# Kernel tuning notes

Measured on AMD Instinct MI355X. Metric: run time of the kernel, lower is better.

## Reference

```python
import jax, jax.numpy as jnp
import numpy as np

D_MODEL = 1024
N_HEADS = 16
MAX_LAG = 512
D_K = D_MODEL // N_HEADS


def setup_inputs() -> dict:
    key = jax.random.key(0)
    ks = jax.random.split(key, 11)
    B, S = 2, 2048
    x = jax.random.normal(ks[0], (B, S, D_MODEL), dtype=jnp.float32)
    lag = jax.random.randint(ks[1], (S,), 0, MAX_LAG + 1, dtype=jnp.int64)
    scale = 1.0 / np.sqrt(D_MODEL)
    wq = jax.random.normal(ks[2], (D_MODEL, D_MODEL), dtype=jnp.float32) * scale
    bq = jnp.zeros((D_MODEL,), dtype=jnp.float32)
    wk = jax.random.normal(ks[3], (D_MODEL, D_MODEL), dtype=jnp.float32) * scale
    bk = jnp.zeros((D_MODEL,), dtype=jnp.float32)
    wv = jax.random.normal(ks[4], (D_MODEL, D_MODEL), dtype=jnp.float32) * scale
    bv = jnp.zeros((D_MODEL,), dtype=jnp.float32)
    wo = jax.random.normal(ks[5], (D_MODEL, D_MODEL), dtype=jnp.float32) * scale
    bo = jnp.zeros((D_MODEL,), dtype=jnp.float32)
    lag_bias = jax.random.normal(ks[6], (N_HEADS, MAX_LAG + 1), dtype=jnp.float32) * 0.02
    return {"x": x, "lag": lag, "wq": wq, "bq": bq, "wk": wk, "bk": bk,
            "wv": wv, "bv": bv, "wo": wo, "bo": bo, "lag_bias": lag_bias}


def reference(x, lag, wq, bq, wk, bk, wv, bv, wo, bo, lag_bias):
    B, S, D = x.shape
    H, dk = N_HEADS, D_K
    # projections: torch Linear is x @ W.T + b; here weights stored as (in, out)
    q = (x @ wq + bq).reshape(B, S, H, dk).transpose(0, 2, 1, 3)  # (B,H,S,dk)
    k = (x @ wk + bk).reshape(B, S, H, dk).transpose(0, 2, 1, 3)
    v = (x @ wv + bv).reshape(B, S, H, dk).transpose(0, 2, 1, 3)
    scores = jnp.einsum('bhqd,bhkd->bhqk', q, k) / jnp.sqrt(jnp.float32(dk))
    ld = jnp.abs(lag[:, None] - lag[None, :]).astype(jnp.int32)  # (S,S)
    bias = lag_bias[:, ld]  # (H,S,S)
    attn = jax.nn.softmax(scores + bias[None], axis=-1)
    out = jnp.einsum('bhqk,bhkd->bhqd', attn, v)
    out = out.transpose(0, 2, 1, 3).reshape(B, S, D)
    return out @ wo + bo
```

## Files before the change

### kernel.cpp

```cpp
#include <hip/hip_runtime.h>

typedef __bf16 bf16;
typedef __bf16 bf16x8 __attribute__((ext_vector_type(8)));
typedef float f32x4 __attribute__((ext_vector_type(4)));

__device__ __forceinline__ f32x4 mfma16(bf16x8 a, bf16x8 b, f32x4 c) {
  return __builtin_amdgcn_mfma_f32_16x16x32_bf16(a, b, c, 0, 0, 0);
}
__device__ __forceinline__ void gload16(const bf16* g, bf16* l) {
  __builtin_amdgcn_global_load_lds((const __attribute__((address_space(1))) unsigned int*)g,
                                   (__attribute__((address_space(3))) unsigned int*)l, 16, 0, 0);
}

__global__ __launch_bounds__(256) void cvt_x_kernel(const float* __restrict__ in,
                                                    bf16* __restrict__ out, int n8) {
  int i = blockIdx.x * 256 + threadIdx.x;
  if (i >= n8) return;
  const float4* p = (const float4*)in + (size_t)i * 2;
  float4 f0 = p[0], f1 = p[1];
  bf16x8 o;
  o[0] = (bf16)f0.x; o[1] = (bf16)f0.y; o[2] = (bf16)f0.z; o[3] = (bf16)f0.w;
  o[4] = (bf16)f1.x; o[5] = (bf16)f1.y; o[6] = (bf16)f1.z; o[7] = (bf16)f1.w;
  *((bf16x8*)out + i) = o;
}

__global__ __launch_bounds__(256) void cvt_wtb_kernel(
    const float* __restrict__ wq, const float* __restrict__ wk,
    const float* __restrict__ wv, const float* __restrict__ wo,
    const float* __restrict__ bq, const float* __restrict__ bk,
    const float* __restrict__ bv, bf16* __restrict__ wqkvt,
    bf16* __restrict__ wot, float* __restrict__ bqkv) {
  int blk = blockIdx.x;
  int tid = threadIdx.x;
  if (blk >= 1024) {
    int i = (blk - 1024) * 256 + tid;
    if (i < 1024) bqkv[i] = bq[i];
    else if (i < 2048) bqkv[i] = bk[i - 1024];
    else if (i < 3072) bqkv[i] = bv[i - 2048];
    return;
  }
  __shared__ float t[64][68];
  int wsel = blk >> 8, sub = blk & 255;
  const float* in = wsel == 0 ? wq : wsel == 1 ? wk : wsel == 2 ? wv : wo;
  bf16* out = (wsel == 3) ? wot : (wqkvt + (size_t)wsel * (1u << 20));
  int bx = sub & 15;
  int by = sub >> 4;
  int r = tid >> 2, p = tid & 3;
  const float* src = in + (size_t)(by * 64 + r) * 1024 + bx * 64 + p * 16;
#pragma unroll
  for (int j = 0; j < 16; j += 4)
    *(float4*)&t[r][p * 16 + j] = *(const float4*)(src + j);
  __syncthreads();
  int n = tid >> 2, sp = tid & 3;
  bf16 tmp[16];
#pragma unroll
  for (int j = 0; j < 16; ++j) tmp[j] = (bf16)t[sp * 16 + j][n];
  bf16* dst = out + (size_t)(bx * 64 + n) * 1024 + by * 64 + sp * 16;
  *(bf16x8*)dst = *(bf16x8*)&tmp[0];
  *(bf16x8*)(dst + 8) = *(bf16x8*)&tmp[8];
}

__global__ __launch_bounds__(256) void sort_lag_kernel(const int* __restrict__ lag,
                                                       int* __restrict__ perm,
                                                       int* __restrict__ slag) {
  __shared__ int l[2048];
  int tid = threadIdx.x;
  for (int i = tid; i < 2048; i += 256) l[i] = lag[i];
  __syncthreads();
  int i = blockIdx.x * 32 + (tid >> 3);
  int s = tid & 7;
  int vi = l[i];
  int cnt = 0;
  for (int j = s * 256; j < s * 256 + 256; j += 4) {
    int4 vj = *(const int4*)&l[j];
    cnt += (vj.x < vi || (vj.x == vi && (j + 0) < i));
    cnt += (vj.y < vi || (vj.y == vi && (j + 1) < i));
    cnt += (vj.z < vi || (vj.z == vi && (j + 2) < i));
    cnt += (vj.w < vi || (vj.w == vi && (j + 3) < i));
  }
  cnt += __shfl_xor(cnt, 1);
  cnt += __shfl_xor(cnt, 2);
  cnt += __shfl_xor(cnt, 4);
  if (s == 0) { perm[cnt] = i; slag[cnt] = vi; }
}

__global__ __launch_bounds__(256) void pack_kv_kernel(const bf16* __restrict__ qkv,
                                                      const int* __restrict__ perm,
                                                      bf16* __restrict__ kp,
                                                      bf16* __restrict__ vt) {
  __shared__ bf16 t[64][72];
  int blk = blockIdx.x;
  int st = blk & 31, h = (blk >> 5) & 15, b = blk >> 9;
  int tid = threadIdx.x;
  int r = tid >> 2, p = tid & 3;
  int src_s = perm[st * 64 + r];
  {
    const bf16* src = qkv + (size_t)(b * 2048 + src_s) * 3072 + 1024 + h * 64 + p * 16;
    bf16* dst = kp + (size_t)((b * 16 + h) * 2048 + st * 64 + r) * 64 + p * 16;
    *(bf16x8*)dst = *(const bf16x8*)src;
    *(bf16x8*)(dst + 8) = *(const bf16x8*)(src + 8);
  }
  {
    const bf16* src = qkv + (size_t)(b * 2048 + src_s) * 3072 + 2048 + h * 64 + p * 16;
    *(bf16x8*)&t[r][p * 16] = *(const bf16x8*)src;
    *(bf16x8*)&t[r][p * 16 + 8] = *(const bf16x8*)(src + 8);
    __syncthreads();
    int d = tid >> 2, sp = tid & 3;
    bf16 tmp[16];
#pragma unroll
    for (int j = 0; j < 16; ++j) tmp[j] = t[sp * 16 + j][d];
    bf16* dst = vt + (size_t)((b * 16 + h) * 64 + d) * 2048 + st * 64 + sp * 16;
    *(bf16x8*)dst = *(bf16x8*)&tmp[0];
    *(bf16x8*)(dst + 8) = *(bf16x8*)&tmp[8];
  }
}

template <int OUT_BF16>
__global__ __launch_bounds__(256) void gemm_bt_kernel(
    const bf16* __restrict__ A, const bf16* __restrict__ Bt,
    const float* __restrict__ bias, void* __restrict__ C,
    int M, int N, int K, int scale_cols, float scale_val) {
  __shared__ __align__(16) bf16 As[128 * 64];
  __shared__ __align__(16) bf16 Bs[128 * 64];
  int bn = blockIdx.x * 128, bm = blockIdx.y * 128;
  int tid = threadIdx.x;
  int l = tid & 63;
  int w = tid >> 6;
  int wr = w >> 1, wc = w & 1;
  int g = l >> 4, c = l & 15;
  int swz = (c & 7) << 3;
  int srow = l >> 3;
  int scol = ((l & 7) ^ srow) << 3;
  const bf16* Ap = A + (size_t)(bm + w * 32 + srow) * K + scol;
  const bf16* Bp = Bt + (size_t)(bn + w * 32 + srow) * K + scol;
  bf16* AsW = As + w * 32 * 64;
  bf16* BsW = Bs + w * 32 * 64;

  f32x4 acc[4][4] = {};
  for (int k0 = 0; k0 < K; k0 += 64) {
    __syncthreads();
#pragma unroll
    for (int i = 0; i < 4; ++i) {
      gload16(Ap + (size_t)(8 * i) * K + k0, AsW + i * 512);
      gload16(Bp + (size_t)(8 * i) * K + k0, BsW + i * 512);
    }
    __syncthreads();
#pragma unroll
    for (int kh = 0; kh < 2; ++kh) {
      bf16x8 af[4], bfr[4];
#pragma unroll
      for (int m = 0; m < 4; ++m)
        af[m] = *(const bf16x8*)&As[(wr * 64 + m * 16 + c) * 64 + ((kh * 32 + g * 8) ^ swz)];
#pragma unroll
      for (int n = 0; n < 4; ++n)
        bfr[n] = *(const bf16x8*)&Bs[(wc * 64 + n * 16 + c) * 64 + ((kh * 32 + g * 8) ^ swz)];
#pragma unroll
      for (int m = 0; m < 4; ++m)
#pragma unroll
        for (int n = 0; n < 4; ++n)
          acc[m][n] = mfma16(af[m], bfr[n], acc[m][n]);
    }
  }
  int rowb = bm + wr * 64;
  int colb = bn + wc * 64;
#pragma unroll
  for (int n = 0; n < 4; ++n) {
    int col = colb + n * 16 + c;
    float bv = bias[col];
    float s = (col < scale_cols) ? scale_val : 1.0f;
#pragma unroll
    for (int m = 0; m < 4; ++m) {
      int row = rowb + m * 16 + g * 4;
#pragma unroll
      for (int j = 0; j < 4; ++j) {
        float v = (acc[m][n][j] + bv) * s;
        if (OUT_BF16)
          ((bf16*)C)[(size_t)(row + j) * N + col] = (bf16)v;
        else
          ((float*)C)[(size_t)(row + j) * N + col] = v;
      }
    }
  }
}

__global__ __launch_bounds__(256) void attn_kernel(
    const bf16* __restrict__ qkv, const bf16* __restrict__ kp,
    const bf16* __restrict__ vt, const int* __restrict__ lag,
    const int* __restrict__ slag, const float* __restrict__ lag_bias,
    bf16* __restrict__ out) {
  __shared__ __align__(16) bf16 Ks0[64 * 64];
  __shared__ __align__(16) bf16 Vs0[64 * 64];
  __shared__ __align__(16) bf16 Ks1[64 * 64];
  __shared__ __align__(16) bf16 Vs1[64 * 64];
  __shared__ __align__(16) bf16 Ps[4][16][72];
  __shared__ float bias_s[516];
  __shared__ int lag_s[2048];

  int blk = blockIdx.x;
  blk = (blk & 7) * 128 + (blk >> 3);
  int qt = blk & 31;
  int h = (blk >> 5) & 15;
  int b = blk >> 9;
  int tid = threadIdx.x;
  int w = tid >> 6, l = tid & 63, g = l >> 4, c = l & 15;

  for (int i = tid; i < 513; i += 256) bias_s[i] = lag_bias[h * 513 + i] * 1.44269504f;
  for (int i = tid; i < 2048; i += 256) lag_s[i] = slag[i];

  int q0 = qt * 64 + w * 16;
  const bf16* qbase = qkv + (size_t)(b * 2048 + q0) * 3072 + h * 64;
  bf16x8 qf[2];
  qf[0] = *(const bf16x8*)(qbase + (size_t)c * 3072 + g * 8);
  qf[1] = *(const bf16x8*)(qbase + (size_t)c * 3072 + 32 + g * 8);

  int lagq[4];
#pragma unroll
  for (int j = 0; j < 4; ++j) lagq[j] = lag[q0 + g * 4 + j];

  int swz = (c & 7) << 3;
  int off0 = (g * 8) ^ swz;
  int off1 = off0 ^ 32;

  int r0 = w * 16 + (l >> 3);
  int colE = ((l & 7) ^ (l >> 3)) << 3;
  const bf16* kbase = kp + (size_t)(b * 16 + h) * 2048 * 64;
  const bf16* vbase = vt + (size_t)(b * 16 + h) * 64 * 2048;
  const bf16* kg0 = kbase + (size_t)r0 * 64 + colE;
  const bf16* kg1 = kbase + (size_t)(r0 + 8) * 64 + colE;
  const bf16* vg0 = vbase + (size_t)r0 * 2048 + colE;
  const bf16* vg1 = vbase + (size_t)(r0 + 8) * 2048 + colE;

#define STAGE(KD, VD)                    \
  do {                                   \
    gload16(kg0, KD + w * 1024);         \
    gload16(kg1, KD + w * 1024 + 512);   \
    gload16(vg0, VD + w * 1024);         \
    gload16(vg1, VD + w * 1024 + 512);   \
    kg0 += 64 * 64; kg1 += 64 * 64;      \
    vg0 += 64; vg1 += 64;                \
  } while (0)

  STAGE(Ks0, Vs0);
  __syncthreads();

  f32x4 oacc[4] = {};
  float psum[4] = {0.f, 0.f, 0.f, 0.f};

#define TILE(KB, VB, KT)                                                          \
  do {                                                                            \
    f32x4 sf[4] = {};                                                             \
    int lagk[4];                                                                  \
    _Pragma("unroll") for (int kb = 0; kb < 4; ++kb) {                            \
      int row = kb * 16 + c;                                                      \
      bf16x8 k0 = *(const bf16x8*)&KB[row * 64 + off0];                           \
      bf16x8 k1 = *(const bf16x8*)&KB[row * 64 + off1];                           \
      sf[kb] = mfma16(qf[0], k0, sf[kb]);                                         \
      sf[kb] = mfma16(qf[1], k1, sf[kb]);                                         \
      lagk[kb] = lag_s[(KT) + kb * 16 + c];                                       \
    }                                                                             \
    _Pragma("unroll") for (int kb = 0; kb < 4; ++kb)                              \
    _Pragma("unroll") for (int j = 0; j < 4; ++j) {                               \
      int ld = lagq[j] - lagk[kb];                                                \
      ld = ld < 0 ? -ld : ld;                                                     \
      float p = __builtin_amdgcn_exp2f(sf[kb][j] + bias_s[ld]);                   \
      psum[j] += p;                                                               \
      Ps[w][g * 4 + j][kb * 16 + c] = (bf16)p;                                    \
    }                                                                             \
    asm volatile("s_waitcnt lgkmcnt(0)" ::: "memory");                            \
    bf16x8 pa0 = *(const bf16x8*)&Ps[w][c][g * 8];                                \
    bf16x8 pa1 = *(const bf16x8*)&Ps[w][c][32 + g * 8];                           \
    _Pragma("unroll") for (int n = 0; n < 4; ++n) {                               \
      int row = n * 16 + c;                                                       \
      bf16x8 v0 = *(const bf16x8*)&VB[row * 64 + off0];                           \
      bf16x8 v1 = *(const bf16x8*)&VB[row * 64 + off1];                           \
      oacc[n] = mfma16(pa0, v0, oacc[n]);                                         \
      oacc[n] = mfma16(pa1, v1, oacc[n]);                                         \
    }                                                                             \
  } while (0)

  for (int kt = 0; kt < 2048; kt += 128) {
    if (kt + 64 < 2048) STAGE(Ks1, Vs1);
    TILE(Ks0, Vs0, kt);
    __syncthreads();
    if (kt + 128 < 2048) STAGE(Ks0, Vs0);
    TILE(Ks1, Vs1, kt + 64);
    __syncthreads();
  }

#pragma unroll
  for (int j = 0; j < 4; ++j) {
    float s = psum[j];
    s += __shfl_xor(s, 1);
    s += __shfl_xor(s, 2);
    s += __shfl_xor(s, 4);
    s += __shfl_xor(s, 8);
    float inv = 1.f / s;
    bf16* ob = out + (size_t)(b * 2048 + q0 + g * 4 + j) * 1024 + h * 64;
#pragma unroll
    for (int n = 0; n < 4; ++n)
      ob[n * 16 + c] = (bf16)(oacc[n][j] * inv);
  }
#undef STAGE
#undef TILE
}

extern "C" void kernel_launch(void* const* d_in, const int* in_sizes, int n_in,
                              void* d_out, int out_size, void* d_ws, size_t ws_size,
                              hipStream_t stream) {
  const float* x        = (const float*)d_in[0];
  const int*   lag      = (const int*)d_in[1];
  const float* wq       = (const float*)d_in[2];
  const float* bq       = (const float*)d_in[3];
  const float* wk       = (const float*)d_in[4];
  const float* bk       = (const float*)d_in[5];
  const float* wv       = (const float*)d_in[6];
  const float* bv       = (const float*)d_in[7];
  const float* wo       = (const float*)d_in[8];
  const float* bo       = (const float*)d_in[9];
  const float* lag_bias = (const float*)d_in[10];

  char* ws = (char*)d_ws;
  bf16*  xb    = (bf16*)ws;
  bf16*  wqkvt = (bf16*)(ws + (8u  << 20));
  bf16*  wot   = (bf16*)(ws + (14u << 20));
  float* bqkv  = (float*)(ws + (16u << 20));
  int*   perm  = (int*)(ws + (16u << 20) + 32768);
  int*   slag  = (int*)(ws + (16u << 20) + 65536);
  bf16*  qkv   = (bf16*)(ws + (17u << 20));
  bf16*  vtb   = (bf16*)(ws + (41u << 20));
  bf16*  aout  = (bf16*)(ws + (49u << 20));
  bf16*  kpk   = xb;

  sort_lag_kernel<<<64, 256, 0, stream>>>(lag, perm, slag);
  cvt_x_kernel<<<2048, 256, 0, stream>>>(x, xb, 524288);
  cvt_wtb_kernel<<<1036, 256, 0, stream>>>(wq, wk, wv, wo, bq, bk, bv, wqkvt, wot, bqkv);
  gemm_bt_kernel<1><<<dim3(24, 32), 256, 0, stream>>>(
      xb, wqkvt, bqkv, qkv, 4096, 3072, 1024, 1024, 0.125f * 1.44269504f);
  pack_kv_kernel<<<1024, 256, 0, stream>>>(qkv, perm, kpk, vtb);
  attn_kernel<<<1024, 256, 0, stream>>>(qkv, kpk, vtb, lag, slag, lag_bias, aout);
  gemm_bt_kernel<0><<<dim3(8, 32), 256, 0, stream>>>(
      aout, wot, bo, (float*)d_out, 4096, 1024, 1024, 0, 1.0f);
}
```

Before: 179.5 us.

## Load K/V fragments directly from global memory instead of LDS double-buffering

The attention kernel drops the double-buffered LDS staging of K and V tiles, and the LDS copy of the sorted lag array. Each lane now reads its MFMA K and V fragments and lag values straight from global memory, relying on L1/L2 caching, and the block-wide barriers inside the loop are removed. With LDS use down to the P scratch and bias table, the launch bounds request four blocks per CU to raise occupancy. The cost is redundant global/cache traffic, since all four waves load the same K/V, and exposed memory latency without explicit prefetch.

New measurement: 327.9 us. 82.7% more time.

```diff
diff --git a/kernel.cpp b/kernel.cpp
--- a/kernel.cpp
+++ b/kernel.cpp
@@ -183,18 +183,13 @@
   }
 }
 
-__global__ __launch_bounds__(256) void attn_kernel(
+__global__ __launch_bounds__(256, 4) void attn_kernel(
     const bf16* __restrict__ qkv, const bf16* __restrict__ kp,
     const bf16* __restrict__ vt, const int* __restrict__ lag,
     const int* __restrict__ slag, const float* __restrict__ lag_bias,
     bf16* __restrict__ out) {
-  __shared__ __align__(16) bf16 Ks0[64 * 64];
-  __shared__ __align__(16) bf16 Vs0[64 * 64];
-  __shared__ __align__(16) bf16 Ks1[64 * 64];
-  __shared__ __align__(16) bf16 Vs1[64 * 64];
   __shared__ __align__(16) bf16 Ps[4][16][72];
   __shared__ float bias_s[516];
-  __shared__ int lag_s[2048];
 
   int blk = blockIdx.x;
   blk = (blk & 7) * 128 + (blk >> 3);
@@ -205,7 +200,6 @@
   int w = tid >> 6, l = tid & 63, g = l >> 4, c = l & 15;
 
   for (int i = tid; i < 513; i += 256) bias_s[i] = lag_bias[h * 513 + i] * 1.44269504f;
-  for (int i = tid; i < 2048; i += 256) lag_s[i] = slag[i];
 
   int q0 = qt * 64 + w * 16;
   const bf16* qbase = qkv + (size_t)(b * 2048 + q0) * 3072 + h * 64;
@@ -217,74 +211,54 @@
 #pragma unroll
   for (int j = 0; j < 4; ++j) lagq[j] = lag[q0 + g * 4 + j];
 
-  int swz = (c & 7) << 3;
-  int off0 = (g * 8) ^ swz;
-  int off1 = off0 ^ 32;
-
-  int r0 = w * 16 + (l >> 3);
-  int colE = ((l & 7) ^ (l >> 3)) << 3;
-  const bf16* kbase = kp + (size_t)(b * 16 + h) * 2048 * 64;
-  const bf16* vbase = vt + (size_t)(b * 16 + h) * 64 * 2048;
-  const bf16* kg0 = kbase + (size_t)r0 * 64 + colE;
-  const bf16* kg1 = kbase + (size_t)(r0 + 8) * 64 + colE;
-  const bf16* vg0 = vbase + (size_t)r0 * 2048 + colE;
-  const bf16* vg1 = vbase + (size_t)(r0 + 8) * 2048 + colE;
-
-#define STAGE(KD, VD)                    \
-  do {                                   \
-    gload16(kg0, KD + w * 1024);         \
-    gload16(kg1, KD + w * 1024 + 512);   \
-    gload16(vg0, VD + w * 1024);         \
-    gload16(vg1, VD + w * 1024 + 512);   \
-    kg0 += 64 * 64; kg1 += 64 * 64;      \
-    vg0 += 64; vg1 += 64;                \
-  } while (0)
-
-  STAGE(Ks0, Vs0);
+  const bf16* krow = kp + (size_t)(b * 16 + h) * 2048 * 64 + (size_t)c * 64 + g * 8;
+  const bf16* vrow[4];
+#pragma unroll
+  for (int n = 0; n < 4; ++n)
+    vrow[n] = vt + (size_t)((b * 16 + h) * 64 + n * 16 + c) * 2048 + g * 8;
+  const int* lagp = slag + c;
+
   __syncthreads();
 
   f32x4 oacc[4] = {};
   float psum[4] = {0.f, 0.f, 0.f, 0.f};
 
-#define TILE(KB, VB, KT)                                                          \
-  do {                                                                            \
-    f32x4 sf[4] = {};                                                             \
-    int lagk[4];                                                                  \
-    _Pragma("unroll") for (int kb = 0; kb < 4; ++kb) {                            \
-      int row = kb * 16 + c;                                                      \
-      bf16x8 k0 = *(const bf16x8*)&KB[row * 64 + off0];                           \
-      bf16x8 k1 = *(const bf16x8*)&KB[row * 64 + off1];                           \
-      sf[kb] = mfma16(qf[0], k0, sf[kb]);                                         \
-      sf[kb] = mfma16(qf[1], k1, sf[kb]);                                         \
-      lagk[kb] = lag_s[(KT) + kb * 16 + c];                                       \
-    }                                                                             \
-    _Pragma("unroll") for (int kb = 0; kb < 4; ++kb)                              \
-    _Pragma("unroll") for (int j = 0; j < 4; ++j) {                               \
-      int ld = lagq[j] - lagk[kb];                                                \
-      ld = ld < 0 ? -ld : ld;                                                     \
-      float p = __builtin_amdgcn_exp2f(sf[kb][j] + bias_s[ld]);                   \
-      psum[j] += p;                                                               \
-      Ps[w][g * 4 + j][kb * 16 + c] = (bf16)p;                                    \
-    }                                                                             \
-    asm volatile("s_waitcnt lgkmcnt(0)" ::: "memory");                            \
-    bf16x8 pa0 = *(const bf16x8*)&Ps[w][c][g * 8];                                \
-    bf16x8 pa1 = *(const bf16x8*)&Ps[w][c][32 + g * 8];                           \
-    _Pragma("unroll") for (int n = 0; n < 4; ++n) {                               \
-      int row = n * 16 + c;                                                       \
-      bf16x8 v0 = *(const bf16x8*)&VB[row * 64 + off0];                           \
-      bf16x8 v1 = *(const bf16x8*)&VB[row * 64 + off1];                           \
-      oacc[n] = mfma16(pa0, v0, oacc[n]);                                         \
-      oacc[n] = mfma16(pa1, v1, oacc[n]);                                         \
-    }                                                                             \
-  } while (0)
-
-  for (int kt = 0; kt < 2048; kt += 128) {
-    if (kt + 64 < 2048) STAGE(Ks1, Vs1);
-    TILE(Ks0, Vs0, kt);
-    __syncthreads();
-    if (kt + 128 < 2048) STAGE(Ks0, Vs0);
-    TILE(Ks1, Vs1, kt + 64);
-    __syncthreads();
+  for (int kt = 0; kt < 2048; kt += 64) {
+    int lagk[4];
+#pragma unroll
+    for (int kb = 0; kb < 4; ++kb) lagk[kb] = lagp[kt + kb * 16];
+
+    f32x4 sf[4] = {};
+    const bf16* kt_base = krow + (size_t)kt * 64;
+#pragma unroll
+    for (int kb = 0; kb < 4; ++kb) {
+      bf16x8 k0 = *(const bf16x8*)(kt_base + kb * 1024);
+      bf16x8 k1 = *(const bf16x8*)(kt_base + kb * 1024 + 32);
+      sf[kb] = mfma16(qf[0], k0, sf[kb]);
+      sf[kb] = mfma16(qf[1], k1, sf[kb]);
+    }
+
+#pragma unroll
+    for (int kb = 0; kb < 4; ++kb) {
+#pragma unroll
+      for (int j = 0; j < 4; ++j) {
+        int ld = lagq[j] - lagk[kb];
+        ld = ld < 0 ? -ld : ld;
+        float p = __builtin_amdgcn_exp2f(sf[kb][j] + bias_s[ld]);
+        psum[j] += p;
+        Ps[w][g * 4 + j][kb * 16 + c] = (bf16)p;
+      }
+    }
+    asm volatile("s_waitcnt lgkmcnt(0)" ::: "memory");
+    bf16x8 pa0 = *(const bf16x8*)&Ps[w][c][g * 8];
+    bf16x8 pa1 = *(const bf16x8*)&Ps[w][c][32 + g * 8];
+#pragma unroll
+    for (int n = 0; n < 4; ++n) {
+      bf16x8 v0 = *(const bf16x8*)(vrow[n] + kt);
+      bf16x8 v1 = *(const bf16x8*)(vrow[n] + kt + 32);
+      oacc[n] = mfma16(pa0, v0, oacc[n]);
+      oacc[n] = mfma16(pa1, v1, oacc[n]);
+    }
   }
 
 #pragma unroll
@@ -300,8 +274,6 @@
     for (int n = 0; n < 4; ++n)
       ob[n * 16 + c] = (bf16)(oacc[n][j] * inv);
   }
-#undef STAGE
-#undef TILE
 }
 
 extern "C" void kernel_launch(void* const* d_in, const int* in_sizes, int n_in,
```
